# Optimization experiments

Measured on AMD Instinct MI355X. Metric: run time of the kernel, lower is better.

## Reference

```python
import jax, jax.numpy as jnp
import numpy as np

N = 50000       # nodes per batched graph
E = 800000      # edges per batched graph
G = 256         # graphs per batch (for max-node pooling)
VOCAB = 120     # node types == embedding vocab
D_EMB = 32
D_H = 100
D_FC = 32
MIN_TYPE = 5    # min_type_count in compute_node_pair_mmd
CAP = 25        # max_nodes_per_type (deterministic: first CAP nodes per type)
KER_MUL = 2.0   # standard multi-kernel Gaussian MMD settings
KER_NUM = 5


def setup_inputs() -> dict:
    key = jax.random.key(0)
    ks = jax.random.split(key, 16)
    ri = lambda k, sh, hi: jax.random.randint(k, sh, 0, hi, dtype=jnp.int32)
    feat = ri(ks[0], (N,), VOCAB)
    feat_src = ri(ks[1], (N,), VOCAB)
    feat_tar = ri(ks[2], (N,), VOCAB)
    edge_index = ri(ks[3], (2, E), N)
    edge_index_src = ri(ks[4], (2, E), N)
    edge_index_tar = ri(ks[5], (2, E), N)
    graph_ids = (jnp.arange(N, dtype=jnp.int32) * G) // N  # sorted, even partition
    mask = (jax.random.uniform(ks[6], (N,)) > 0.1).astype(jnp.float32)
    embed = jax.random.normal(ks[7], (VOCAB, D_EMB)) * 0.02
    gcn_w = jax.random.normal(ks[8], (D_EMB, D_H)) * (1.0 / np.sqrt(D_EMB))
    gcn_b = jnp.zeros((D_H,), jnp.float32)
    fc_w = jax.random.normal(ks[9], (D_H, D_FC)) * (1.0 / np.sqrt(D_H))
    fc_b = jnp.zeros((D_FC,), jnp.float32)
    def_w = jax.random.normal(ks[10], (D_FC, 1)) * (1.0 / np.sqrt(D_FC))
    def_b = jnp.zeros((1,), jnp.float32)
    return dict(feat=feat, feat_src=feat_src, feat_tar=feat_tar,
                edge_index=edge_index, edge_index_src=edge_index_src,
                edge_index_tar=edge_index_tar, graph_ids=graph_ids, mask=mask,
                embed=embed, gcn_w=gcn_w, gcn_b=gcn_b, fc_w=fc_w, fc_b=fc_b,
                def_w=def_w, def_b=def_b)


def _graph_conv(x, ei, w, b):
    # DGL GraphConv, norm='both': D_out^{-1/2} A^T D_in^{-1/2} X W + b (degrees clamped to 1)
    src, dst = ei[0], ei[1]
    ones = jnp.ones((ei.shape[1],), x.dtype)
    outdeg = jnp.clip(jax.ops.segment_sum(ones, src, num_segments=N), 1.0)
    indeg = jnp.clip(jax.ops.segment_sum(ones, dst, num_segments=N), 1.0)
    h = (x @ w) * (outdeg ** -0.5)[:, None]          # [N, D_H], weight first (in<=out)
    agg = jax.ops.segment_sum(h[src], dst, num_segments=N)
    return agg * (indeg ** -0.5)[:, None] + b


def _mmd(src_types, tgt_types, src_feats, tgt_feats):
    # per-type multi-kernel Gaussian MMD; deterministic cap of CAP nodes/type
    def per_type(t):
        sm = (src_types == t)
        tm = (tgt_types == t)
        s_cnt = sm.sum()
        t_cnt = tm.sum()
        sv, si = jax.lax.top_k(sm.astype(jnp.float32), CAP)  # first CAP indices of type t
        tv, ti = jax.lax.top_k(tm.astype(jnp.float32), CAP)
        X = jnp.concatenate([src_feats[si], tgt_feats[ti]], 0)      # [2C, D]
        valid = jnp.concatenate([sv, tv]) > 0                        # [2C]
        pm = valid[:, None] & valid[None, :]
        D2 = jnp.sum((X[:, None, :] - X[None, :, :]) ** 2, -1)      # [2C, 2C]
        m = jnp.minimum(s_cnt, CAP).astype(jnp.float32)
        n = jnp.minimum(t_cnt, CAP).astype(jnp.float32)
        ntot = m + n
        bw = jnp.sum(jnp.where(pm, D2, 0.0)) / jnp.maximum(ntot * ntot - ntot, 1.0)
        bw = bw / (KER_MUL ** (KER_NUM // 2))
        bws = bw * (KER_MUL ** jnp.arange(KER_NUM, dtype=jnp.float32))
        K = jnp.sum(jnp.exp(-D2[None] / jnp.maximum(bws, 1e-8)[:, None, None]), 0)
        K = jnp.where(pm, K, 0.0)
        XX = K[:CAP, :CAP].sum() / jnp.maximum(m * m, 1.0)
        YY = K[CAP:, CAP:].sum() / jnp.maximum(n * n, 1.0)
        XY = K[:CAP, CAP:].sum() / jnp.maximum(m * n, 1.0)
        loss = XX + YY - 2.0 * XY
        inc = (s_cnt >= MIN_TYPE) & (t_cnt >= MIN_TYPE)
        return jnp.where(inc, loss, 0.0), inc.astype(jnp.float32)
    losses, incs = jax.vmap(per_type)(jnp.arange(1, VOCAB, dtype=jnp.int32))  # type 0 skipped
    cnt = incs.sum()
    return jnp.where(cnt > 0, losses.sum() / jnp.maximum(cnt, 1.0), 0.0)


def reference(feat, feat_src, feat_tar, edge_index, edge_index_src, edge_index_tar,
              graph_ids, mask, embed, gcn_w, gcn_b, fc_w, fc_b, def_w, def_b):
    def process(f, ei, msk):
        x = embed[f]
        if msk is not None:
            x = x * msk[:, None]
        h = jax.nn.relu(_graph_conv(x, ei, gcn_w, gcn_b))            # node feats 'h'
        pooled = jax.ops.segment_max(h, graph_ids, num_segments=G,
                                     indices_are_sorted=True)        # dgl.max_nodes
        return h, pooled

    _, pool = process(feat, edge_index, mask)
    h_src, pool_src = process(feat_src, edge_index_src, None)
    h_tar, pool_tar = process(feat_tar, edge_index_tar, None)

    x_batch_mmd = pool @ fc_w + fc_b        # [G, 32]
    x_src_mmd = pool_src @ fc_w + fc_b
    x_tar_mmd = pool_tar @ fc_w + fc_b
    src_node_feat = h_src @ fc_w + fc_b     # [N, 32]
    tgt_node_feat = h_tar @ fc_w + fc_b
    x_loss_mmd_node = _mmd(feat_src, feat_tar, src_node_feat, tgt_node_feat)
    defect_prob = jax.nn.sigmoid(x_batch_mmd @ def_w + def_b)  # [G, 1]
    # domain_clf output is not returned by the original forward, so it is skipped here.
    return (x_batch_mmd, defect_prob, x_src_mmd, x_tar_mmd, x_loss_mmd_node)
```

## Files before the change

kernel.cpp:

```cpp
#include <hip/hip_runtime.h>
#include <hip/hip_bf16.h>

#define Nn 50000
#define Ee 800000
#define Gg 256
#define VOC 120
#define DH 100
#define CAPc 25
#define NTYPE 119
#define NCHUNK 196
#define DR 4
#define DS 32
#define DWORDS 6250
#define NBIN 391
#define EBLK 782

#define P1_T 0
#define P1_SEL 120
#define P1_BIN 512
#define P1_DEG 2858
#define P1_PCLR 3242
#define P1_SCLR 3317
#define P1_TOT 3415
#define P3_SELG 0
#define P3_BSC 392
#define P3_DMG 2738
#define P3_TOT 3031

__global__ __launch_bounds__(256) void prep_kernel(
        const float* __restrict__ embed, const float* __restrict__ gcn_w, float* __restrict__ Tp,
        const int* __restrict__ feat_src, const int* __restrict__ feat_tar,
        int* __restrict__ chunkcnt,
        const int* __restrict__ ei0, const int* __restrict__ ei1, const int* __restrict__ ei2,
        int* __restrict__ cntbuf, int* __restrict__ partial,
        float* __restrict__ pool, int* __restrict__ selpos, float* __restrict__ stats) {
    __shared__ int sm[DWORDS];
    int bx = blockIdx.x;
    int tid = threadIdx.x;

    if (bx < P1_SEL) {
        int t = bx - P1_T;
        if (tid < DH) {
            float acc = 0.f;
#pragma unroll
            for (int k = 0; k < 32; ++k) acc = fmaf(embed[t * 32 + k], gcn_w[k * DH + tid], acc);
            Tp[t * DH + tid] = acc;
        }
        return;
    }
    if (bx < P1_BIN) {
        int idx = bx - P1_SEL;
        int side = idx / NCHUNK, chunk = idx - side * NCHUNK;
        const int* f = side ? feat_tar : feat_src;
        if (tid < VOC) sm[tid] = 0;
        __syncthreads();
        int i = chunk * 256 + tid;
        if (i < Nn) atomicAdd(&sm[f[i]], 1);
        __syncthreads();
        if (tid < VOC) chunkcnt[(side * NCHUNK + chunk) * VOC + tid] = sm[tid];
        return;
    }
    if (bx < P1_DEG) {
        int idx = bx - P1_BIN;
        int g = idx / EBLK, blk = idx - g * EBLK;
        const int* dst = ((g == 0) ? ei0 : (g == 1) ? ei1 : ei2) + Ee;
        for (int i = tid; i < NBIN; i += 256) sm[i] = 0;
        __syncthreads();
        int e0 = (blk * 256 + tid) * 4;
        if (e0 < Ee) {
            uint4 d = *(const uint4*)&dst[e0];
            atomicAdd(&sm[d.x >> 7], 1);
            atomicAdd(&sm[d.y >> 7], 1);
            atomicAdd(&sm[d.z >> 7], 1);
            atomicAdd(&sm[d.w >> 7], 1);
        }
        __syncthreads();
        int* outp = cntbuf + ((size_t)blk * 3 + g) * NBIN;
        for (int i = tid; i < NBIN; i += 256) outp[i] = sm[i];
        return;
    }
    if (bx < P1_PCLR) {
        int idx = bx - P1_DEG;
        int g = idx / (DR * DS), rs = idx - g * (DR * DS);
        int r = rs & (DR - 1), s = rs >> 2;
        const int* ei = (g == 0) ? ei0 : (g == 1) ? ei1 : ei2;
        const uint4* a4 = (const uint4*)(ei + s * (Ee / DS));
        for (int i = tid; i < DWORDS; i += 256) sm[i] = 0;
        __syncthreads();
        unsigned base = r * (2 * DWORDS);
        for (int idx2 = tid; idx2 < (Ee / DS) / 4; idx2 += 256) {
            uint4 v = a4[idx2];
            unsigned q;
            q = v.x - base; if (q < 2 * DWORDS) atomicAdd(&sm[q >> 1], 1 << ((q & 1) * 16));
            q = v.y - base; if (q < 2 * DWORDS) atomicAdd(&sm[q >> 1], 1 << ((q & 1) * 16));
            q = v.z - base; if (q < 2 * DWORDS) atomicAdd(&sm[q >> 1], 1 << ((q & 1) * 16));
            q = v.w - base; if (q < 2 * DWORDS) atomicAdd(&sm[q >> 1], 1 << ((q & 1) * 16));
        }
        __syncthreads();
        int* outp = partial + ((size_t)(g * DR + r) * DS + s) * DWORDS;
        for (int i = tid; i < DWORDS; i += 256) outp[i] = sm[i];
        return;
    }
    if (bx < P1_SCLR) {
        int i = (bx - P1_PCLR) * 256 + tid;
        ((float4*)pool)[i] = make_float4(0.f, 0.f, 0.f, 0.f);
        return;
    }
    {
        int b = bx - P1_SCLR;
        int i = b * 256 + tid;
        if (i < 25000) ((int4*)selpos)[i] = make_int4(-1, -1, -1, -1);
        if (b == 0 && tid == 0) {
            stats[0] = 0.f;
            ((int*)stats)[1] = 0;
            ((int*)stats)[2] = 0;
        }
        return;
    }
}

__global__ __launch_bounds__(64) void prefix_kernel(const int* __restrict__ chunkcnt,
                                                    int* __restrict__ baseb,
                                                    int* __restrict__ fullcnt,
                                                    const int* __restrict__ cntbuf,
                                                    int* __restrict__ ofsbuf,
                                                    int* __restrict__ bintot) {
    int bx = blockIdx.x;
    int lane = threadIdx.x;
    if (bx < 2 * VOC) {
        int side = bx / VOC, t = bx - side * VOC;
        int run = 0;
        for (int c0 = 0; c0 < NCHUNK; c0 += 64) {
            int c = c0 + lane;
            int v = (c < NCHUNK) ? chunkcnt[(side * NCHUNK + c) * VOC + t] : 0;
            int inc = v;
#pragma unroll
            for (int o = 1; o < 64; o <<= 1) {
                int u = __shfl_up(inc, o, 64);
                if (lane >= o) inc += u;
            }
            if (c < NCHUNK) baseb[(side * NCHUNK + c) * VOC + t] = run + inc - v;
            run += __shfl(inc, 63, 64);
        }
        if (lane == 0) fullcnt[side * VOC + t] = run;
    } else {
        int pair = bx - 2 * VOC;
        int g = pair / NBIN, bin = pair - g * NBIN;
        int run = 0;
        for (int c0 = 0; c0 < EBLK; c0 += 64) {
            int c = c0 + lane;
            int v = (c < EBLK) ? cntbuf[((size_t)c * 3 + g) * NBIN + bin] : 0;
            int inc = v;
#pragma unroll
            for (int o = 1; o < 64; o <<= 1) {
                int u = __shfl_up(inc, o, 64);
                if (lane >= o) inc += u;
            }
            if (c < EBLK) ofsbuf[((size_t)c * 3 + g) * NBIN + bin] = run + inc - v;
            run += __shfl(inc, 63, 64);
        }
        if (lane == 0) bintot[pair] = run;
    }
}

__global__ __launch_bounds__(64) void binbase_kernel(const int* __restrict__ bintot,
                                                     int* __restrict__ binbase) {
    int g = blockIdx.x;
    int lane = threadIdx.x;
    int run = 0;
    for (int c0 = 0; c0 < NBIN; c0 += 64) {
        int c = c0 + lane;
        int v = (c < NBIN) ? bintot[g * NBIN + c] : 0;
        int inc = v;
#pragma unroll
        for (int o = 1; o < 64; o <<= 1) {
            int u = __shfl_up(inc, o, 64);
            if (lane >= o) inc += u;
        }
        if (c < NBIN) binbase[g * NBIN + c] = run + inc - v;
        run += __shfl(inc, 63, 64);
    }
}

__global__ __launch_bounds__(256) void scatter_kernel(
        const int* __restrict__ feat_src, const int* __restrict__ feat_tar,
        const int* __restrict__ baseb, int* __restrict__ selpos_src, int* __restrict__ selpos_tar,
        const int* __restrict__ ei0, const int* __restrict__ ei1, const int* __restrict__ ei2,
        const int* __restrict__ ofsbuf, const int* __restrict__ binbase,
        unsigned* __restrict__ ebuf,
        const int* __restrict__ partial, const int* __restrict__ feat0,
        const float* __restrict__ mask, float2* __restrict__ pc) {
    __shared__ int sm[NBIN];
    int bx = blockIdx.x;
    int tid = threadIdx.x;

    if (bx < P3_BSC) {
        int idx = bx - P3_SELG;
        int side = idx / NCHUNK, chunk = idx - side * NCHUNK;
        const int* f = side ? feat_tar : feat_src;
        int* selpos = side ? selpos_tar : selpos_src;
        int i = chunk * 256 + tid;
        int t = (i < Nn) ? f[i] : -1;
        sm[tid] = t;
        int bv = 0;
        bool need = (t >= 1);
        if (need) {
            bv = baseb[(side * NCHUNK + chunk) * VOC + t];
            need = (bv < CAPc);
        }
        int any = __syncthreads_count((int)need);
        if (any == 0) return;
        if (need) {
            int rank = bv;
            for (int q = 0; q < 256; ++q)
                if (q < tid && sm[q] == t) rank++;
            if (rank < CAPc) selpos[i] = (t - 1) * CAPc + rank;
        }
        return;
    }
    if (bx < P3_DMG) {
        int idx = bx - P3_BSC;
        int g = idx / EBLK, blk = idx - g * EBLK;
        const int* ei = (g == 0) ? ei0 : (g == 1) ? ei1 : ei2;
        const int* ofp = ofsbuf + ((size_t)blk * 3 + g) * NBIN;
        for (int i = tid; i < NBIN; i += 256)
            sm[i] = binbase[g * NBIN + i] + ofp[i];
        __syncthreads();
        unsigned* eb = ebuf + (size_t)g * Ee;
        int e0 = (blk * 256 + tid) * 4;
        if (e0 < Ee) {
            uint4 s = *(const uint4*)&ei[e0];
            uint4 d = *(const uint4*)&ei[Ee + e0];
            int p;
            p = atomicAdd(&sm[d.x >> 7], 1); eb[p] = ((d.x & 127u) << 16) | s.x;
            p = atomicAdd(&sm[d.y >> 7], 1); eb[p] = ((d.y & 127u) << 16) | s.y;
            p = atomicAdd(&sm[d.z >> 7], 1); eb[p] = ((d.z & 127u) << 16) | s.z;
            p = atomicAdd(&sm[d.w >> 7], 1); eb[p] = ((d.w & 127u) << 16) | s.w;
        }
        return;
    }
    {
        int idx = (bx - P3_DMG) * 256 + tid;
        if (idx >= 3 * DR * DWORDS) return;
        int g = idx / (DR * DWORDS);
        int rem = idx - g * (DR * DWORDS);
        int r = rem / DWORDS, w = rem - r * DWORDS;
        const int* p = partial + ((size_t)(g * DR + r) * DS) * DWORDS + w;
        int sum = 0;
#pragma unroll 8
        for (int s = 0; s < DS; ++s) sum += p[s * DWORDS];
        int c0 = sum & 0xFFFF, c1 = sum >> 16;
        int n0 = r * (2 * DWORDS) + 2 * w;
        const int* ft = (g == 0) ? feat0 : (g == 1) ? feat_src : feat_tar;
        float cf0 = rsqrtf((float)max(c0, 1));
        float cf1 = rsqrtf((float)max(c1, 1));
        if (g == 0) {
            cf0 *= mask[n0];
            cf1 *= mask[n0 + 1];
        }
        float4 v = make_float4(cf0, __int_as_float(ft[n0]), cf1, __int_as_float(ft[n0 + 1]));
        ((float4*)(pc + (size_t)g * Nn))[r * DWORDS + w] = v;
        return;
    }
}

__global__ __launch_bounds__(256, 2) void fused_wh_kernel(const unsigned* __restrict__ ebuf,
                                                          const float2* __restrict__ pc,
                                                          const int* __restrict__ binbase,
                                                          const int* __restrict__ bintot,
                                                          const float* __restrict__ Tp,
                                                          const int* __restrict__ selposall,
                                                          float* __restrict__ h_sel,
                                                          const float* __restrict__ gcn_b,
                                                          float* __restrict__ pool) {
    __shared__ float Wl[VOC * 128];
    __shared__ int cnt[128];
    int g = blockIdx.y, bin = blockIdx.x;
    int tid = threadIdx.x;

    float4* Wl4 = (float4*)Wl;
#pragma unroll
    for (int i = 0; i < 15; ++i) Wl4[tid + i * 256] = make_float4(0.f, 0.f, 0.f, 0.f);
    if (tid < 128) cnt[tid] = 0;
    __syncthreads();

    int base = binbase[g * NBIN + bin];
    int n = bintot[g * NBIN + bin];
    const unsigned* eb = ebuf + (size_t)g * Ee + base;
    const float2* pcg = pc + (size_t)g * Nn;
    for (int i = tid; i < n; i += 256) {
        unsigned e = eb[i];
        float2 p = pcg[e & 0xFFFFu];
        int dl = e >> 16;
        atomicAdd(&Wl[__float_as_int(p.y) * 128 + dl], p.x);
        atomicAdd(&cnt[dl], 1);
    }
    __syncthreads();

    int lane = tid & 63, wv = tid >> 6;
    int chcol = __builtin_amdgcn_readfirstlane(wv) * 25;
    const float* Tc = Tp + chcol;
    int r0 = bin * 128;
    int nr = min(128, Nn - r0);
    float accA[25], accB[25];
#pragma unroll
    for (int j = 0; j < 25; ++j) { accA[j] = 0.f; accB[j] = 0.f; }

    __builtin_amdgcn_s_setprio(1);
    for (int t0 = 0; t0 < VOC; t0 += 8) {
        float wA8[8], wB8[8];
#pragma unroll
        for (int u = 0; u < 8; ++u) {
            wA8[u] = Wl[(t0 + u) * 128 + lane];
            wB8[u] = Wl[(t0 + u) * 128 + lane + 64];
        }
#pragma unroll
        for (int u = 0; u < 8; ++u) {
            const float* tr = Tc + (t0 + u) * DH;
#pragma unroll
            for (int j = 0; j < 25; ++j) {
                float tv = tr[j];
                accA[j] = fmaf(wA8[u], tv, accA[j]);
                accB[j] = fmaf(wB8[u], tv, accB[j]);
            }
        }
    }
    __builtin_amdgcn_s_setprio(0);

    int rA = lane, rB = lane + 64;
    bool vA = rA < nr, vB = rB < nr;
    float rsA = vA ? rsqrtf((float)max(cnt[rA], 1)) : 0.f;
    float rsB = vB ? rsqrtf((float)max(cnt[rB], 1)) : 0.f;
    int growA = r0 + rA, growB = r0 + rB;
    int seg0 = (r0 * Gg) / Nn;
    int segA = (growA * Gg) / Nn, segB = (growB * Gg) / Nn;
    float bb[25];
#pragma unroll
    for (int j = 0; j < 25; ++j) bb[j] = gcn_b[wv * 25 + j];

    float v0[25], v1[25];
#pragma unroll
    for (int j = 0; j < 25; ++j) {
        float hA = vA ? fmaxf(fmaf(accA[j], rsA, bb[j]), 0.f) : 0.f;
        float hB = vB ? fmaxf(fmaf(accB[j], rsB, bb[j]), 0.f) : 0.f;
        accA[j] = hA;
        accB[j] = hB;
        v0[j] = fmaxf((vA && segA == seg0) ? hA : 0.f, (vB && segB == seg0) ? hB : 0.f);
        v1[j] = fmaxf((vA && segA != seg0) ? hA : 0.f, (vB && segB != seg0) ? hB : 0.f);
    }
#pragma unroll
    for (int m = 1; m < 64; m <<= 1) {
#pragma unroll
        for (int j = 0; j < 25; ++j) {
            v0[j] = fmaxf(v0[j], __shfl_xor(v0[j], m, 64));
            v1[j] = fmaxf(v1[j], __shfl_xor(v1[j], m, 64));
        }
    }
    if (lane == 0) {
        float* poolg = pool + g * (Gg * DH) + seg0 * DH + wv * 25;
        for (int j = 0; j < 25; ++j) atomicMax((int*)&poolg[j], __float_as_int(v0[j]));
        int segLast = ((r0 + nr - 1) * Gg) / Nn;
        if (segLast != seg0)
            for (int j = 0; j < 25; ++j) atomicMax((int*)&poolg[DH + j], __float_as_int(v1[j]));
    }

    if (g > 0) {
        const int* selpos = selposall + (size_t)(g - 1) * Nn;
        float* hs = h_sel + (size_t)(g == 2 ? NTYPE * CAPc * DH : 0);
        int spA = vA ? selpos[growA] : -1;
        int spB = vB ? selpos[growB] : -1;
        if (spA >= 0) {
            float* d = hs + (size_t)spA * DH + wv * 25;
            for (int j = 0; j < 25; ++j) d[j] = accA[j];
        }
        if (spB >= 0) {
            float* d = hs + (size_t)spB * DH + wv * 25;
            for (int j = 0; j < 25; ++j) d[j] = accB[j];
        }
    }
}

__global__ __launch_bounds__(256) void post_kernel(const float* __restrict__ pool,
                                                   const float* __restrict__ fc_w,
                                                   const float* __restrict__ fc_b,
                                                   const float* __restrict__ def_w,
                                                   const float* __restrict__ def_b,
                                                   float* __restrict__ out,
                                                   const float* __restrict__ h_sel,
                                                   const int* __restrict__ fullcnt,
                                                   float* __restrict__ X) {
    __shared__ float smf[DH * 32];
    int bx = blockIdx.x;
    int tid = threadIdx.x;
    if (bx < Gg) {
        int g = bx;
        if (tid < 96) {
            int p = tid >> 5, j = tid & 31;
            float acc = fc_b[j];
            const float* pr = pool + p * (Gg * DH) + g * DH;
#pragma unroll 4
            for (int k = 0; k < DH; ++k) acc = fmaf(pr[k], fc_w[k * 32 + j], acc);
            int off = (p == 0) ? 0 : (p == 1 ? 8448 : 16640);
            out[off + g * 32 + j] = acc;
            if (p == 0) smf[j] = acc;
        }
        __syncthreads();
        if (tid < 32) {
            float v = smf[tid] * def_w[tid];
            for (int o = 16; o; o >>= 1) v += __shfl_down(v, o, 64);
            if (tid == 0) out[8192 + g] = 1.f / (1.f + expf(-(v + def_b[0])));
        }
        return;
    }
    {
        int t = bx - Gg;
        for (int i = tid; i < DH * 32; i += 256) smf[i] = fc_w[i];
        __syncthreads();
        int cs = min(fullcnt[t + 1], CAPc);
        int ct = min(fullcnt[VOC + t + 1], CAPc);
        int j = tid & 31, rg = tid >> 5;
        for (int r = rg; r < 2 * CAPc; r += 8) {
            int side = r / CAPc, rr = r % CAPc;
            int cnt = side ? ct : cs;
            float acc = 0.f;
            if (rr < cnt) {
                const float* hr = h_sel + ((size_t)side * NTYPE * CAPc + (size_t)t * CAPc + rr) * DH;
                acc = fc_b[j];
#pragma unroll 4
                for (int k = 0; k < DH; ++k) acc = fmaf(hr[k], smf[k * 32 + j], acc);
            }
            X[(size_t)t * 1600 + r * 32 + j] = acc;
        }
        return;
    }
}

__device__ __forceinline__ float block_reduce256(float v, float* red, int tid) {
    __syncthreads();
    red[tid] = v;
    __syncthreads();
    for (int s = 128; s > 0; s >>= 1) {
        if (tid < s) red[tid] += red[tid + s];
        __syncthreads();
    }
    return red[0];
}

__global__ __launch_bounds__(256) void mmd_kernel(const float* __restrict__ X,
                                                  const int* __restrict__ fullcnt,
                                                  float* __restrict__ stats,
                                                  float* __restrict__ out) {
    int t = blockIdx.x;
    __shared__ float Xs[50 * 32];
    __shared__ float D2[50 * 50];
    __shared__ float red[256];
    int tid = threadIdx.x;
    for (int i = tid; i < 1600; i += 256) Xs[i] = X[(size_t)t * 1600 + i];
    __syncthreads();
    int scF = fullcnt[t + 1];
    int tcF = fullcnt[VOC + t + 1];
    int m = min(scF, CAPc), n2 = min(tcF, CAPc);
    float bwpart = 0.f;
    for (int idx = tid; idx < 2500; idx += 256) {
        int i = idx / 50, j = idx % 50;
        float d = 0.f;
#pragma unroll
        for (int k = 0; k < 32; ++k) {
            float df = Xs[i * 32 + k] - Xs[j * 32 + k];
            d = fmaf(df, df, d);
        }
        D2[idx] = d;
        bool vi = (i < CAPc) ? (i < m) : (i - CAPc < n2);
        bool vj = (j < CAPc) ? (j < m) : (j - CAPc < n2);
        if (vi && vj) bwpart += d;
    }
    float bwsum = block_reduce256(bwpart, red, tid);
    float ntot = (float)(m + n2);
    float bw = bwsum / fmaxf(ntot * ntot - ntot, 1.f) * 0.25f;
    float bws[5];
#pragma unroll
    for (int k = 0; k < 5; ++k) bws[k] = fmaxf(bw * (float)(1 << k), 1e-8f);
    float xx = 0.f, yy = 0.f, xy = 0.f;
    for (int idx = tid; idx < 2500; idx += 256) {
        int i = idx / 50, j = idx % 50;
        bool vi = (i < CAPc) ? (i < m) : (i - CAPc < n2);
        bool vj = (j < CAPc) ? (j < m) : (j - CAPc < n2);
        if (!(vi && vj)) continue;
        float d = D2[idx];
        float kv = 0.f;
#pragma unroll
        for (int k = 0; k < 5; ++k) kv += expf(-d / bws[k]);
        if (i < CAPc && j < CAPc) xx += kv;
        else if (i >= CAPc && j >= CAPc) yy += kv;
        else if (i < CAPc) xy += kv;
    }
    float rxx = block_reduce256(xx, red, tid);
    float ryy = block_reduce256(yy, red, tid);
    float rxy = block_reduce256(xy, red, tid);
    if (tid == 0) {
        float fm = (float)m, fn = (float)n2;
        float XX = rxx / fmaxf(fm * fm, 1.f);
        float YY = ryy / fmaxf(fn * fn, 1.f);
        float XY = rxy / fmaxf(fm * fn, 1.f);
        float loss = XX + YY - 2.f * XY;
        int inc = (scF >= 5 && tcF >= 5) ? 1 : 0;
        atomicAdd(&stats[0], inc ? loss : 0.f);
        atomicAdd((int*)&stats[1], inc);
        __threadfence();
        int old = atomicAdd((int*)&stats[2], 1);
        if (old == NTYPE - 1) {
            float s = atomicAdd(&stats[0], 0.f);
            int c = atomicAdd((int*)&stats[1], 0);
            out[24832] = (c > 0) ? s / (float)max(c, 1) : 0.f;
        }
    }
}

extern "C" void kernel_launch(void* const* d_in, const int* in_sizes, int n_in,
                              void* d_out, int out_size, void* d_ws, size_t ws_size,
                              hipStream_t stream) {
    const int* feat = (const int*)d_in[0];
    const int* feat_src = (const int*)d_in[1];
    const int* feat_tar = (const int*)d_in[2];
    const int* ei0 = (const int*)d_in[3];
    const int* ei1 = (const int*)d_in[4];
    const int* ei2 = (const int*)d_in[5];
    const float* mask = (const float*)d_in[7];
    const float* embed = (const float*)d_in[8];
    const float* gcn_w = (const float*)d_in[9];
    const float* gcn_b = (const float*)d_in[10];
    const float* fc_w = (const float*)d_in[11];
    const float* fc_b = (const float*)d_in[12];
    const float* def_w = (const float*)d_in[13];
    const float* def_b = (const float*)d_in[14];
    float* out = (float*)d_out;

    char* wsb = (char*)d_ws;
    int* partial = (int*)(wsb + 0);
    float* Tp = (float*)(wsb + 9600000);
    float* pool = (float*)(wsb + 9660000);
    float2* pc = (float2*)(wsb + 9967200);
    int* selpos = (int*)(wsb + 11167200);
    float* h_sel = (float*)(wsb + 11567200);
    int* fullcnt = (int*)(wsb + 13947200);
    float* X = (float*)(wsb + 13948160);
    float* stats = (float*)(wsb + 14709760);
    int* chunkcnt = (int*)(wsb + 14710720);
    int* baseb = (int*)(wsb + 14898880);
    int* cntbuf = (int*)(wsb + 15087040);
    int* ofsbuf = (int*)(wsb + 18756200);
    int* bintot = (int*)(wsb + 22425400);
    int* binbase = (int*)(wsb + 22430400);
    unsigned* ebuf = (unsigned*)(wsb + 22435200);

    prep_kernel<<<P1_TOT, 256, 0, stream>>>(embed, gcn_w, Tp, feat_src, feat_tar, chunkcnt,
                                            ei0, ei1, ei2, cntbuf, partial, pool, selpos, stats);
    prefix_kernel<<<2 * VOC + 3 * NBIN, 64, 0, stream>>>(chunkcnt, baseb, fullcnt, cntbuf,
                                                         ofsbuf, bintot);
    binbase_kernel<<<3, 64, 0, stream>>>(bintot, binbase);
    scatter_kernel<<<P3_TOT, 256, 0, stream>>>(feat_src, feat_tar, baseb, selpos, selpos + Nn,
                                               ei0, ei1, ei2, ofsbuf, binbase, ebuf, partial,
                                               feat, mask, pc);
    fused_wh_kernel<<<dim3(NBIN, 3), 256, 0, stream>>>(ebuf, pc, binbase, bintot, Tp, selpos,
                                                       h_sel, gcn_b, pool);
    post_kernel<<<Gg + NTYPE, 256, 0, stream>>>(pool, fc_w, fc_b, def_w, def_b, out, h_sel,
                                                fullcnt, X);
    mmd_kernel<<<NTYPE, 256, 0, stream>>>(X, fullcnt, stats, out);
}
```

Measured before the change: 214.4 us.

## Move degree-coef pass earlier and pre-gather source coefs into edge buckets

The pass that builds per-node (degree coefficient, type) pairs moves from the scatter kernel into the prefix kernel, now run with 64-thread blocks, so pc exists before edges are bucketed. The scatter kernel then gathers each source's coefficient and type while it bins edges and writes 8-byte records (value, type*128+local dst). The aggregation kernel reads those records directly instead of doing a random gather into pc, at the cost of doubling edge-buffer traffic. The s_setprio hints around the inner FMA loop are removed.

```diff
diff --git a/kernel.cpp b/kernel.cpp
--- a/kernel.cpp
+++ b/kernel.cpp
@@ -22,10 +22,13 @@
 #define P1_PCLR 3242
 #define P1_SCLR 3317
 #define P1_TOT 3415
+#define P2_SELP 0
+#define P2_BINP 240
+#define P2_DMG 1413
+#define P2_TOT 2585
 #define P3_SELG 0
 #define P3_BSC 392
-#define P3_DMG 2738
-#define P3_TOT 3031
+#define P3_TOT 2738
 
 __global__ __launch_bounds__(256) void prep_kernel(
         const float* __restrict__ embed, const float* __restrict__ gcn_w, float* __restrict__ Tp,
@@ -124,10 +127,16 @@
                                                     int* __restrict__ fullcnt,
                                                     const int* __restrict__ cntbuf,
                                                     int* __restrict__ ofsbuf,
-                                                    int* __restrict__ bintot) {
+                                                    int* __restrict__ bintot,
+                                                    const int* __restrict__ partial,
+                                                    const int* __restrict__ feat0,
+                                                    const int* __restrict__ feat_src,
+                                                    const int* __restrict__ feat_tar,
+                                                    const float* __restrict__ mask,
+                                                    float2* __restrict__ pc) {
     int bx = blockIdx.x;
     int lane = threadIdx.x;
-    if (bx < 2 * VOC) {
+    if (bx < P2_BINP) {
         int side = bx / VOC, t = bx - side * VOC;
         int run = 0;
         for (int c0 = 0; c0 < NCHUNK; c0 += 64) {
@@ -143,8 +152,10 @@
             run += __shfl(inc, 63, 64);
         }
         if (lane == 0) fullcnt[side * VOC + t] = run;
-    } else {
-        int pair = bx - 2 * VOC;
+        return;
+    }
+    if (bx < P2_DMG) {
+        int pair = bx - P2_BINP;
         int g = pair / NBIN, bin = pair - g * NBIN;
         int run = 0;
         for (int c0 = 0; c0 < EBLK; c0 += 64) {
@@ -160,87 +171,10 @@
             run += __shfl(inc, 63, 64);
         }
         if (lane == 0) bintot[pair] = run;
-    }
-}
-
-__global__ __launch_bounds__(64) void binbase_kernel(const int* __restrict__ bintot,
-                                                     int* __restrict__ binbase) {
-    int g = blockIdx.x;
-    int lane = threadIdx.x;
-    int run = 0;
-    for (int c0 = 0; c0 < NBIN; c0 += 64) {
-        int c = c0 + lane;
-        int v = (c < NBIN) ? bintot[g * NBIN + c] : 0;
-        int inc = v;
-#pragma unroll
-        for (int o = 1; o < 64; o <<= 1) {
-            int u = __shfl_up(inc, o, 64);
-            if (lane >= o) inc += u;
-        }
-        if (c < NBIN) binbase[g * NBIN + c] = run + inc - v;
-        run += __shfl(inc, 63, 64);
-    }
-}
-
-__global__ __launch_bounds__(256) void scatter_kernel(
-        const int* __restrict__ feat_src, const int* __restrict__ feat_tar,
-        const int* __restrict__ baseb, int* __restrict__ selpos_src, int* __restrict__ selpos_tar,
-        const int* __restrict__ ei0, const int* __restrict__ ei1, const int* __restrict__ ei2,
-        const int* __restrict__ ofsbuf, const int* __restrict__ binbase,
-        unsigned* __restrict__ ebuf,
-        const int* __restrict__ partial, const int* __restrict__ feat0,
-        const float* __restrict__ mask, float2* __restrict__ pc) {
-    __shared__ int sm[NBIN];
-    int bx = blockIdx.x;
-    int tid = threadIdx.x;
-
-    if (bx < P3_BSC) {
-        int idx = bx - P3_SELG;
-        int side = idx / NCHUNK, chunk = idx - side * NCHUNK;
-        const int* f = side ? feat_tar : feat_src;
-        int* selpos = side ? selpos_tar : selpos_src;
-        int i = chunk * 256 + tid;
-        int t = (i < Nn) ? f[i] : -1;
-        sm[tid] = t;
-        int bv = 0;
-        bool need = (t >= 1);
-        if (need) {
-            bv = baseb[(side * NCHUNK + chunk) * VOC + t];
-            need = (bv < CAPc);
-        }
-        int any = __syncthreads_count((int)need);
-        if (any == 0) return;
-        if (need) {
-            int rank = bv;
-            for (int q = 0; q < 256; ++q)
-                if (q < tid && sm[q] == t) rank++;
-            if (rank < CAPc) selpos[i] = (t - 1) * CAPc + rank;
-        }
-        return;
-    }
-    if (bx < P3_DMG) {
-        int idx = bx - P3_BSC;
-        int g = idx / EBLK, blk = idx - g * EBLK;
-        const int* ei = (g == 0) ? ei0 : (g == 1) ? ei1 : ei2;
-        const int* ofp = ofsbuf + ((size_t)blk * 3 + g) * NBIN;
-        for (int i = tid; i < NBIN; i += 256)
-            sm[i] = binbase[g * NBIN + i] + ofp[i];
-        __syncthreads();
-        unsigned* eb = ebuf + (size_t)g * Ee;
-        int e0 = (blk * 256 + tid) * 4;
-        if (e0 < Ee) {
-            uint4 s = *(const uint4*)&ei[e0];
-            uint4 d = *(const uint4*)&ei[Ee + e0];
-            int p;
-            p = atomicAdd(&sm[d.x >> 7], 1); eb[p] = ((d.x & 127u) << 16) | s.x;
-            p = atomicAdd(&sm[d.y >> 7], 1); eb[p] = ((d.y & 127u) << 16) | s.y;
-            p = atomicAdd(&sm[d.z >> 7], 1); eb[p] = ((d.z & 127u) << 16) | s.z;
-            p = atomicAdd(&sm[d.w >> 7], 1); eb[p] = ((d.w & 127u) << 16) | s.w;
-        }
         return;
     }
     {
-        int idx = (bx - P3_DMG) * 256 + tid;
+        int idx = (bx - P2_DMG) * 64 + lane;
         if (idx >= 3 * DR * DWORDS) return;
         int g = idx / (DR * DWORDS);
         int rem = idx - g * (DR * DWORDS);
@@ -264,8 +198,92 @@
     }
 }
 
-__global__ __launch_bounds__(256, 2) void fused_wh_kernel(const unsigned* __restrict__ ebuf,
-                                                          const float2* __restrict__ pc,
+__global__ __launch_bounds__(64) void binbase_kernel(const int* __restrict__ bintot,
+                                                     int* __restrict__ binbase) {
+    int g = blockIdx.x;
+    int lane = threadIdx.x;
+    int run = 0;
+    for (int c0 = 0; c0 < NBIN; c0 += 64) {
+        int c = c0 + lane;
+        int v = (c < NBIN) ? bintot[g * NBIN + c] : 0;
+        int inc = v;
+#pragma unroll
+        for (int o = 1; o < 64; o <<= 1) {
+            int u = __shfl_up(inc, o, 64);
+            if (lane >= o) inc += u;
+        }
+        if (c < NBIN) binbase[g * NBIN + c] = run + inc - v;
+        run += __shfl(inc, 63, 64);
+    }
+}
+
+__global__ __launch_bounds__(256) void scatter_kernel(
+        const int* __restrict__ feat_src, const int* __restrict__ feat_tar,
+        const int* __restrict__ baseb, int* __restrict__ selpos_src, int* __restrict__ selpos_tar,
+        const int* __restrict__ ei0, const int* __restrict__ ei1, const int* __restrict__ ei2,
+        const int* __restrict__ ofsbuf, const int* __restrict__ binbase,
+        uint2* __restrict__ ebuf, const float2* __restrict__ pc) {
+    __shared__ int sm[NBIN];
+    int bx = blockIdx.x;
+    int tid = threadIdx.x;
+
+    if (bx < P3_BSC) {
+        int idx = bx - P3_SELG;
+        int side = idx / NCHUNK, chunk = idx - side * NCHUNK;
+        const int* f = side ? feat_tar : feat_src;
+        int* selpos = side ? selpos_tar : selpos_src;
+        int i = chunk * 256 + tid;
+        int t = (i < Nn) ? f[i] : -1;
+        sm[tid] = t;
+        int bv = 0;
+        bool need = (t >= 1);
+        if (need) {
+            bv = baseb[(side * NCHUNK + chunk) * VOC + t];
+            need = (bv < CAPc);
+        }
+        int any = __syncthreads_count((int)need);
+        if (any == 0) return;
+        if (need) {
+            int rank = bv;
+            for (int q = 0; q < 256; ++q)
+                if (q < tid && sm[q] == t) rank++;
+            if (rank < CAPc) selpos[i] = (t - 1) * CAPc + rank;
+        }
+        return;
+    }
+    {
+        int idx = bx - P3_BSC;
+        int g = idx / EBLK, blk = idx - g * EBLK;
+        const int* ei = (g == 0) ? ei0 : (g == 1) ? ei1 : ei2;
+        const int* ofp = ofsbuf + ((size_t)blk * 3 + g) * NBIN;
+        for (int i = tid; i < NBIN; i += 256)
+            sm[i] = binbase[g * NBIN + i] + ofp[i];
+        __syncthreads();
+        const float2* pcg = pc + (size_t)g * Nn;
+        uint2* eb = ebuf + (size_t)g * Ee;
+        int e0 = (blk * 256 + tid) * 4;
+        if (e0 < Ee) {
+            uint4 s = *(const uint4*)&ei[e0];
+            uint4 d = *(const uint4*)&ei[Ee + e0];
+            float2 p0 = pcg[s.x];
+            float2 p1 = pcg[s.y];
+            float2 p2 = pcg[s.z];
+            float2 p3 = pcg[s.w];
+            int p;
+            p = atomicAdd(&sm[d.x >> 7], 1);
+            eb[p] = make_uint2(__float_as_uint(p0.x), __float_as_int(p0.y) * 128 + (d.x & 127u));
+            p = atomicAdd(&sm[d.y >> 7], 1);
+            eb[p] = make_uint2(__float_as_uint(p1.x), __float_as_int(p1.y) * 128 + (d.y & 127u));
+            p = atomicAdd(&sm[d.z >> 7], 1);
+            eb[p] = make_uint2(__float_as_uint(p2.x), __float_as_int(p2.y) * 128 + (d.z & 127u));
+            p = atomicAdd(&sm[d.w >> 7], 1);
+            eb[p] = make_uint2(__float_as_uint(p3.x), __float_as_int(p3.y) * 128 + (d.w & 127u));
+        }
+        return;
+    }
+}
+
+__global__ __launch_bounds__(256, 2) void fused_wh_kernel(const uint2* __restrict__ ebuf,
                                                           const int* __restrict__ binbase,
                                                           const int* __restrict__ bintot,
                                                           const float* __restrict__ Tp,
@@ -286,14 +304,11 @@
 
     int base = binbase[g * NBIN + bin];
     int n = bintot[g * NBIN + bin];
-    const unsigned* eb = ebuf + (size_t)g * Ee + base;
-    const float2* pcg = pc + (size_t)g * Nn;
+    const uint2* eb = ebuf + (size_t)g * Ee + base;
     for (int i = tid; i < n; i += 256) {
-        unsigned e = eb[i];
-        float2 p = pcg[e & 0xFFFFu];
-        int dl = e >> 16;
-        atomicAdd(&Wl[__float_as_int(p.y) * 128 + dl], p.x);
-        atomicAdd(&cnt[dl], 1);
+        uint2 e = eb[i];
+        atomicAdd(&Wl[e.y], __uint_as_float(e.x));
+        atomicAdd(&cnt[e.y & 127u], 1);
     }
     __syncthreads();
 
@@ -306,7 +321,6 @@
 #pragma unroll
     for (int j = 0; j < 25; ++j) { accA[j] = 0.f; accB[j] = 0.f; }
 
-    __builtin_amdgcn_s_setprio(1);
     for (int t0 = 0; t0 < VOC; t0 += 8) {
         float wA8[8], wB8[8];
 #pragma unroll
@@ -325,7 +339,6 @@
             }
         }
     }
-    __builtin_amdgcn_s_setprio(0);
 
     int rA = lane, rB = lane + 64;
     bool vA = rA < nr, vB = rB < nr;
@@ -551,17 +564,16 @@
     int* ofsbuf = (int*)(wsb + 18756200);
     int* bintot = (int*)(wsb + 22425400);
     int* binbase = (int*)(wsb + 22430400);
-    unsigned* ebuf = (unsigned*)(wsb + 22435200);
+    uint2* ebuf = (uint2*)(wsb + 22435200);
 
     prep_kernel<<<P1_TOT, 256, 0, stream>>>(embed, gcn_w, Tp, feat_src, feat_tar, chunkcnt,
                                             ei0, ei1, ei2, cntbuf, partial, pool, selpos, stats);
-    prefix_kernel<<<2 * VOC + 3 * NBIN, 64, 0, stream>>>(chunkcnt, baseb, fullcnt, cntbuf,
-                                                         ofsbuf, bintot);
+    prefix_kernel<<<P2_TOT, 64, 0, stream>>>(chunkcnt, baseb, fullcnt, cntbuf, ofsbuf, bintot,
+                                             partial, feat, feat_src, feat_tar, mask, pc);
     binbase_kernel<<<3, 64, 0, stream>>>(bintot, binbase);
     scatter_kernel<<<P3_TOT, 256, 0, stream>>>(feat_src, feat_tar, baseb, selpos, selpos + Nn,
-                                               ei0, ei1, ei2, ofsbuf, binbase, ebuf, partial,
-                                               feat, mask, pc);
-    fused_wh_kernel<<<dim3(NBIN, 3), 256, 0, stream>>>(ebuf, pc, binbase, bintot, Tp, selpos,
+                                               ei0, ei1, ei2, ofsbuf, binbase, ebuf, pc);
+    fused_wh_kernel<<<dim3(NBIN, 3), 256, 0, stream>>>(ebuf, binbase, bintot, Tp, selpos,
                                                        h_sel, gcn_b, pool);
     post_kernel<<<Gg + NTYPE, 256, 0, stream>>>(pool, fc_w, fc_b, def_w, def_b, out, h_sel,
                                                 fullcnt, X);
```

Result: no change. 215.0 us (+0.3%).
